# Optimization experiments

Hardware: AMD Instinct MI355X
Metric: run time of the kernel (lower is better)

Reference implementation:

```python
import jax, jax.numpy as jnp
import numpy as np

B, T, D, H = 256, 1024, 128, 256
SHIFT = 1


def setup_inputs() -> dict:
    key = jax.random.key(0)
    ks = jax.random.split(key, 16)

    def w(k, shp):
        return jax.random.normal(k, shp, dtype=jnp.float32) / np.float32(np.sqrt(shp[0]))

    return {
        "x": jax.random.normal(ks[0], (B, T, D), dtype=jnp.float32),
        "Wx": w(ks[1], (D, H)), "bx": jnp.zeros((H,), jnp.float32),
        "W1": w(ks[2], (D, 100)), "b1": jnp.zeros((100,), jnp.float32),
        "W2": w(ks[3], (100, 100)), "b2": jnp.zeros((100,), jnp.float32),
        "W3": w(ks[4], (100, 100)), "b3": jnp.zeros((100,), jnp.float32),
        "W4": w(ks[5], (100, 50)), "b4": jnp.zeros((50,), jnp.float32),
        "W5": w(ks[6], (50, H)), "b5": jnp.zeros((H,), jnp.float32),
        "Wo": w(ks[7], (H, 1)), "bo": jnp.zeros((1,), jnp.float32),
        "shift": SHIFT,
    }


def reference(x, Wx, bx, W1, b1, W2, b2, W3, b3, W4, b4, W5, b5, Wo, bo, shift):
    # x: [B, T, D] -> time-major [T, B, D] (matches input.permute(1,0,2))
    xs = jnp.swapaxes(x, 0, 1)
    # Input-dependent parts are independent of hidden state: batch them over time.
    lin_x = xs @ Wx + bx                       # [T, B, H]
    h = jax.nn.relu(xs @ W1 + b1)
    h = jax.nn.relu(h @ W2 + b2)
    h = jax.nn.relu(h @ W3 + b3)
    h = jax.nn.relu(h @ W4 + b4)
    fx = jax.nn.sigmoid(h @ W5 + b5)           # [T, B, H]
    gate = fx * jax.nn.sigmoid(lin_x)          # [T, B, H]

    def step(hid, bt):
        hid = jax.nn.relu(jnp.roll(hid, shift, axis=-1) + bt)
        return hid, None

    hidden0 = jnp.zeros((x.shape[0], Wx.shape[1]), dtype=x.dtype)
    hidden, _ = jax.lax.scan(step, hidden0, gate)
    output = jax.nn.sigmoid(hidden @ Wo + bo)  # [B, 1]
    return (output, hidden)
```

## Files before the change

### kernel.cpp

```cpp
#include <hip/hip_runtime.h>
#include <math.h>

#define B_N 256
#define T_N 1024
#define D_N 128
#define H_N 256

#define SPS 120

#define SP_OFF  0
#define SQ_OFF  7680
#define GUARD_OFF 15360
#define ACC_OFF 15368
#define SMEM_SH 15880

typedef __attribute__((ext_vector_type(8))) short short8;
typedef __attribute__((ext_vector_type(4))) float f32x4;

#define WXT_OFF 0
#define W1T_OFF 32768
#define W2T_OFF 47104
#define W3T_OFF 61440
#define W4T_OFF 75776
#define W5T_OFF 83968
#define WT_TOTAL 100352

__device__ __forceinline__ float sigmoid_f(float z) {
    return 1.0f / (1.0f + __expf(-z));
}
__device__ __forceinline__ unsigned short f2bf(float f) {
    unsigned u = __float_as_uint(f);
    return (unsigned short)((u + 0x7FFFu + ((u >> 16) & 1u)) >> 16);
}

__global__ __launch_bounds__(256) void prep_weights(
    const float* __restrict__ Wx, const float* __restrict__ W1,
    const float* __restrict__ W2, const float* __restrict__ W3,
    const float* __restrict__ W4, const float* __restrict__ W5,
    short* __restrict__ wt)
{
    int idx = blockIdx.x * 256 + threadIdx.x;
    if (idx >= WT_TOTAL) return;
    const float* src; int base, KR, K, N;
    if (idx < W1T_OFF)      { src = Wx; base = WXT_OFF; KR = 4; K = 128; N = 256; }
    else if (idx < W2T_OFF) { src = W1; base = W1T_OFF; KR = 4; K = 128; N = 100; }
    else if (idx < W3T_OFF) { src = W2; base = W2T_OFF; KR = 4; K = 100; N = 100; }
    else if (idx < W4T_OFF) { src = W3; base = W3T_OFF; KR = 4; K = 100; N = 100; }
    else if (idx < W5T_OFF) { src = W4; base = W4T_OFF; KR = 4; K = 100; N =  50; }
    else                    { src = W5; base = W5T_OFF; KR = 2; K =  50; N = 256; }
    int e    = idx - base;
    int j    = e & 7;
    int slot = e >> 3;
    int lane = slot & 63;
    int kk   = slot >> 6;
    int k4   = kk & (KR - 1);
    int nt   = kk / KR;
    int n = nt * 16 + (lane & 15);
    int k = k4 * 32 + (lane >> 4) * 8 + j;
    float v = (k < K && n < N) ? src[(size_t)k * N + n] : 0.0f;
    wt[idx] = (short)f2bf(v);
}

template<int STRIDE>
__device__ __forceinline__ void loadA(const short* __restrict__ base, short8 (&a)[4],
                                      int mbase, int lr, int lq)
{
    #pragma unroll
    for (int k = 0; k < 4; ++k)
        a[k] = *reinterpret_cast<const short8*>(&base[(mbase + lr) * STRIDE + k * 32 + lq * 8]);
}

template<int NT, int OUTS>
__device__ __forceinline__ void denseLG(const short8 (&a)[4], const short* __restrict__ gW,
                                        const float* __restrict__ bias, int ncap,
                                        short* __restrict__ dst, int mbase, int lr, int lq,
                                        int lane)
{
    #pragma unroll 2
    for (int nt = 0; nt < NT; ++nt) {
        const int n0 = nt * 16;
        f32x4 acc = {0.f, 0.f, 0.f, 0.f};
        #pragma unroll
        for (int k = 0; k < 4; ++k) {
            const short8 bf = *reinterpret_cast<const short8*>(&gW[((nt * 4 + k) * 64 + lane) * 8]);
            acc = __builtin_amdgcn_mfma_f32_16x16x32_bf16(a[k], bf, acc, 0, 0, 0);
        }
        const bool valid = (n0 + lr < ncap);
        const float bv = valid ? bias[n0 + lr] : 0.0f;
        #pragma unroll
        for (int r = 0; r < 4; ++r) {
            float v = valid ? fmaxf(acc[r] + bv, 0.0f) : 0.0f;
            dst[(mbase + lq * 4 + r) * OUTS + n0 + lr] = (short)f2bf(v);
        }
    }
}

__global__ __launch_bounds__(256, 4) void srnn_gate_scan(
    const float* __restrict__ x, const short* __restrict__ wt,
    const float* __restrict__ bx, const float* __restrict__ b1,
    const float* __restrict__ b2, const float* __restrict__ b3,
    const float* __restrict__ b4, const float* __restrict__ b5,
    const int* __restrict__ shiftp,
    float* __restrict__ out)
{
    __shared__ __align__(16) short smem[SMEM_SH];
    short* sP = smem + SP_OFF;
    short* sQ = smem + SQ_OFF;
    float* accum = reinterpret_cast<float*>(smem + ACC_OFF);

    const int tid  = threadIdx.x;
    const int b    = blockIdx.x & 255;
    const int seg  = blockIdx.x >> 8;
    const int lane = tid & 63;
    const int mbase = (tid >> 6) * 16;
    const int lr = lane & 15;
    const int lq = lane >> 4;
    const int s  = *shiftp;
    const int tw0 = seg * 64 + mbase;

    {
        const float4 z = {0.f, 0.f, 0.f, 0.f};
        float4* dst = reinterpret_cast<float4*>(smem);
        #pragma unroll
        for (int i = 0; i < 8; ++i) {
            int sl = tid + i * 256;
            if (sl < SMEM_SH / 8) dst[sl] = z;
        }
    }

    short8 ax4[4];
    {
        const float* xr = x + ((size_t)b * T_N + tw0 + lr) * D_N;
        #pragma unroll
        for (int k = 0; k < 4; ++k) {
            const float4 v0 = *reinterpret_cast<const float4*>(&xr[k * 32 + lq * 8]);
            const float4 v1 = *reinterpret_cast<const float4*>(&xr[k * 32 + lq * 8 + 4]);
            short8 t;
            t[0] = (short)f2bf(v0.x); t[1] = (short)f2bf(v0.y);
            t[2] = (short)f2bf(v0.z); t[3] = (short)f2bf(v0.w);
            t[4] = (short)f2bf(v1.x); t[5] = (short)f2bf(v1.y);
            t[6] = (short)f2bf(v1.z); t[7] = (short)f2bf(v1.w);
            ax4[k] = t;
        }
    }
    __syncthreads();

    short8 aL[4];
    denseLG<7, SPS>(ax4, wt + W1T_OFF, b1, 100, sP, mbase, lr, lq, lane);
    loadA<SPS>(sP, aL, mbase, lr, lq);
    denseLG<7, SPS>(aL, wt + W2T_OFF, b2, 100, sQ, mbase, lr, lq, lane);
    loadA<SPS>(sQ, aL, mbase, lr, lq);
    denseLG<7, SPS>(aL, wt + W3T_OFF, b3, 100, sP, mbase, lr, lq, lane);
    loadA<SPS>(sP, aL, mbase, lr, lq);
    denseLG<4, SPS>(aL, wt + W4T_OFF, b4, 50, sQ, mbase, lr, lq, lane);

    short8 c0 = *reinterpret_cast<const short8*>(&sQ[(mbase + lr) * SPS + 0 + lq * 8]);
    short8 c1 = *reinterpret_cast<const short8*>(&sQ[(mbase + lr) * SPS + 32 + lq * 8]);

    const short* gWx = wt + WXT_OFF;
    const short* gW5 = wt + W5T_OFF;
    #pragma unroll 2
    for (int ntl = 0; ntl < 16; ++ntl) {
        const int n0 = ntl * 16;
        f32x4 axv = {0.f, 0.f, 0.f, 0.f};
        #pragma unroll
        for (int k = 0; k < 4; ++k) {
            const short8 bf = *reinterpret_cast<const short8*>(&gWx[((ntl * 4 + k) * 64 + lane) * 8]);
            axv = __builtin_amdgcn_mfma_f32_16x16x32_bf16(ax4[k], bf, axv, 0, 0, 0);
        }
        f32x4 a5v = {0.f, 0.f, 0.f, 0.f};
        {
            const short8 bf0 = *reinterpret_cast<const short8*>(&gW5[((ntl * 2 + 0) * 64 + lane) * 8]);
            const short8 bf1 = *reinterpret_cast<const short8*>(&gW5[((ntl * 2 + 1) * 64 + lane) * 8]);
            a5v = __builtin_amdgcn_mfma_f32_16x16x32_bf16(c0, bf0, a5v, 0, 0, 0);
            a5v = __builtin_amdgcn_mfma_f32_16x16x32_bf16(c1, bf1, a5v, 0, 0, 0);
        }
        const float bxv = bx[n0 + lr];
        const float b5v = b5[n0 + lr];
        #pragma unroll
        for (int r = 0; r < 4; ++r) {
            const int t = tw0 + lq * 4 + r;
            const float g = sigmoid_f(a5v[r] + b5v) * sigmoid_f(axv[r] + bxv);
            int v = n0 + lr + s * (T_N - 1 - t);
            v %= H_N; if (v < 0) v += H_N;
            atomicAdd(&accum[v], g);
        }
    }
    __syncthreads();

    atomicAdd(&out[256 + b * 256 + tid], accum[tid]);
}

__global__ __launch_bounds__(256) void srnn_output(
    const float* __restrict__ Wo, const float* __restrict__ bo,
    float* __restrict__ out)
{
    __shared__ float red[256];
    const int b = blockIdx.x, tid = threadIdx.x;
    red[tid] = out[256 + b * 256 + tid] * Wo[tid];
    __syncthreads();
    #pragma unroll
    for (int off = 128; off > 0; off >>= 1) {
        if (tid < off) red[tid] += red[tid + off];
        __syncthreads();
    }
    if (tid == 0) out[b] = sigmoid_f(red[0] + bo[0]);
}

extern "C" void kernel_launch(void* const* d_in, const int* in_sizes, int n_in,
                              void* d_out, int out_size, void* d_ws, size_t ws_size,
                              hipStream_t stream)
{
    const float* x  = (const float*)d_in[0];
    const float* Wx = (const float*)d_in[1];
    const float* bx = (const float*)d_in[2];
    const float* W1 = (const float*)d_in[3];
    const float* b1 = (const float*)d_in[4];
    const float* W2 = (const float*)d_in[5];
    const float* b2 = (const float*)d_in[6];
    const float* W3 = (const float*)d_in[7];
    const float* b3 = (const float*)d_in[8];
    const float* W4 = (const float*)d_in[9];
    const float* b4 = (const float*)d_in[10];
    const float* W5 = (const float*)d_in[11];
    const float* b5 = (const float*)d_in[12];
    const float* Wo = (const float*)d_in[13];
    const float* bo = (const float*)d_in[14];
    const int* shiftp = (const int*)d_in[15];
    float* out = (float*)d_out;
    short* wt  = (short*)d_ws;

    hipMemsetAsync(d_out, 0, (size_t)out_size * sizeof(float), stream);

    prep_weights<<<dim3((WT_TOTAL + 255) / 256), dim3(256), 0, stream>>>(
        Wx, W1, W2, W3, W4, W5, wt);
    srnn_gate_scan<<<dim3(4096), dim3(256), 0, stream>>>(
        x, wt, bx, b1, b2, b3, b4, b5, shiftp, out);
    srnn_output<<<dim3(256), dim3(256), 0, stream>>>(Wo, bo, out);
}
```

Measured before the change: 576.5 us.

## Process two row tiles per wave, fuse output reduction, merge memset into prep

Each wave now handles 32 time rows, so every loaded weight fragment feeds two MFMAs. This halves weight-fragment traffic per row, and the grid is cut to 2048 blocks. The final Wo reduction moves into the scan kernel, where the last-arriving segment block per batch does it after a per-batch atomic counter. The output memset is folded into the weight-prep kernel. The sigmoid product is simplified to one reciprocal and the modulo to a mask. This adds register pressure, a counter in workspace, and a fence-based completion protocol.

New measurement: 699.3 us. 1.21x slower.

```diff
diff --git a/kernel.cpp b/kernel.cpp
--- a/kernel.cpp
+++ b/kernel.cpp
@@ -5,14 +5,12 @@
 #define T_N 1024
 #define D_N 128
 #define H_N 256
+#define NSEG 8
 
 #define SPS 120
-
-#define SP_OFF  0
-#define SQ_OFF  7680
-#define GUARD_OFF 15360
-#define ACC_OFF 15368
-#define SMEM_SH 15880
+#define SACT_SH (4 * 32 * SPS)
+#define ACC_OFF (SACT_SH + 8)
+#define SMEM_SH (ACC_OFF + 512)
 
 typedef __attribute__((ext_vector_type(8))) short short8;
 typedef __attribute__((ext_vector_type(4))) float f32x4;
@@ -33,13 +31,19 @@
     return (unsigned short)((u + 0x7FFFu + ((u >> 16) & 1u)) >> 16);
 }
 
-__global__ __launch_bounds__(256) void prep_weights(
+__global__ __launch_bounds__(256) void prep_init(
     const float* __restrict__ Wx, const float* __restrict__ W1,
     const float* __restrict__ W2, const float* __restrict__ W3,
     const float* __restrict__ W4, const float* __restrict__ W5,
-    short* __restrict__ wt)
+    short* __restrict__ wt, float* __restrict__ out, int* __restrict__ cnt)
 {
     int idx = blockIdx.x * 256 + threadIdx.x;
+    if (idx < 16448) {
+        const float4 z = {0.f, 0.f, 0.f, 0.f};
+        reinterpret_cast<float4*>(out)[idx] = z;
+    } else if (idx < 16448 + 256) {
+        cnt[idx - 16448] = 0;
+    }
     if (idx >= WT_TOTAL) return;
     const float* src; int base, KR, K, N;
     if (idx < W1T_OFF)      { src = Wx; base = WXT_OFF; KR = 4; K = 128; N = 256; }
@@ -61,36 +65,40 @@
     wt[idx] = (short)f2bf(v);
 }
 
-template<int STRIDE>
-__device__ __forceinline__ void loadA(const short* __restrict__ base, short8 (&a)[4],
-                                      int mbase, int lr, int lq)
-{
-    #pragma unroll
-    for (int k = 0; k < 4; ++k)
-        a[k] = *reinterpret_cast<const short8*>(&base[(mbase + lr) * STRIDE + k * 32 + lq * 8]);
-}
-
-template<int NT, int OUTS>
-__device__ __forceinline__ void denseLG(const short8 (&a)[4], const short* __restrict__ gW,
+__device__ __forceinline__ void loadA2(const short* __restrict__ sA, short8 (&a)[2][4],
+                                       int lr, int lq)
+{
+    #pragma unroll
+    for (int rb = 0; rb < 2; ++rb)
+        #pragma unroll
+        for (int k = 0; k < 4; ++k)
+            a[rb][k] = *reinterpret_cast<const short8*>(&sA[(rb * 16 + lr) * SPS + k * 32 + lq * 8]);
+}
+
+template<int NT>
+__device__ __forceinline__ void denseL2(const short8 (&a)[2][4], const short* __restrict__ gW,
                                         const float* __restrict__ bias, int ncap,
-                                        short* __restrict__ dst, int mbase, int lr, int lq,
-                                        int lane)
+                                        short* __restrict__ sA, int lr, int lq, int lane)
 {
     #pragma unroll 2
     for (int nt = 0; nt < NT; ++nt) {
         const int n0 = nt * 16;
-        f32x4 acc = {0.f, 0.f, 0.f, 0.f};
+        f32x4 acc0 = {0.f, 0.f, 0.f, 0.f};
+        f32x4 acc1 = {0.f, 0.f, 0.f, 0.f};
         #pragma unroll
         for (int k = 0; k < 4; ++k) {
             const short8 bf = *reinterpret_cast<const short8*>(&gW[((nt * 4 + k) * 64 + lane) * 8]);
-            acc = __builtin_amdgcn_mfma_f32_16x16x32_bf16(a[k], bf, acc, 0, 0, 0);
+            acc0 = __builtin_amdgcn_mfma_f32_16x16x32_bf16(a[0][k], bf, acc0, 0, 0, 0);
+            acc1 = __builtin_amdgcn_mfma_f32_16x16x32_bf16(a[1][k], bf, acc1, 0, 0, 0);
         }
         const bool valid = (n0 + lr < ncap);
         const float bv = valid ? bias[n0 + lr] : 0.0f;
         #pragma unroll
         for (int r = 0; r < 4; ++r) {
-            float v = valid ? fmaxf(acc[r] + bv, 0.0f) : 0.0f;
-            dst[(mbase + lq * 4 + r) * OUTS + n0 + lr] = (short)f2bf(v);
+            float v0 = valid ? fmaxf(acc0[r] + bv, 0.0f) : 0.0f;
+            float v1 = valid ? fmaxf(acc1[r] + bv, 0.0f) : 0.0f;
+            sA[(lq * 4 + r) * SPS + n0 + lr]        = (short)f2bf(v0);
+            sA[(16 + lq * 4 + r) * SPS + n0 + lr]   = (short)f2bf(v1);
         }
     }
 }
@@ -101,22 +109,23 @@
     const float* __restrict__ b2, const float* __restrict__ b3,
     const float* __restrict__ b4, const float* __restrict__ b5,
     const int* __restrict__ shiftp,
+    const float* __restrict__ Wo, const float* __restrict__ bo,
+    int* __restrict__ cnt,
     float* __restrict__ out)
 {
     __shared__ __align__(16) short smem[SMEM_SH];
-    short* sP = smem + SP_OFF;
-    short* sQ = smem + SQ_OFF;
     float* accum = reinterpret_cast<float*>(smem + ACC_OFF);
 
     const int tid  = threadIdx.x;
     const int b    = blockIdx.x & 255;
     const int seg  = blockIdx.x >> 8;
     const int lane = tid & 63;
-    const int mbase = (tid >> 6) * 16;
+    const int wid  = tid >> 6;
     const int lr = lane & 15;
     const int lq = lane >> 4;
     const int s  = *shiftp;
-    const int tw0 = seg * 64 + mbase;
+    const int tw0 = seg * 128 + wid * 32;
+    short* sA = smem + wid * 32 * SPS;
 
     {
         const float4 z = {0.f, 0.f, 0.f, 0.f};
@@ -128,9 +137,10 @@
         }
     }
 
-    short8 ax4[4];
-    {
-        const float* xr = x + ((size_t)b * T_N + tw0 + lr) * D_N;
+    short8 ax[2][4];
+    #pragma unroll
+    for (int rb = 0; rb < 2; ++rb) {
+        const float* xr = x + ((size_t)b * T_N + tw0 + rb * 16 + lr) * D_N;
         #pragma unroll
         for (int k = 0; k < 4; ++k) {
             const float4 v0 = *reinterpret_cast<const float4*>(&xr[k * 32 + lq * 8]);
@@ -140,71 +150,95 @@
             t[2] = (short)f2bf(v0.z); t[3] = (short)f2bf(v0.w);
             t[4] = (short)f2bf(v1.x); t[5] = (short)f2bf(v1.y);
             t[6] = (short)f2bf(v1.z); t[7] = (short)f2bf(v1.w);
-            ax4[k] = t;
-        }
-    }
-    __syncthreads();
-
-    short8 aL[4];
-    denseLG<7, SPS>(ax4, wt + W1T_OFF, b1, 100, sP, mbase, lr, lq, lane);
-    loadA<SPS>(sP, aL, mbase, lr, lq);
-    denseLG<7, SPS>(aL, wt + W2T_OFF, b2, 100, sQ, mbase, lr, lq, lane);
-    loadA<SPS>(sQ, aL, mbase, lr, lq);
-    denseLG<7, SPS>(aL, wt + W3T_OFF, b3, 100, sP, mbase, lr, lq, lane);
-    loadA<SPS>(sP, aL, mbase, lr, lq);
-    denseLG<4, SPS>(aL, wt + W4T_OFF, b4, 50, sQ, mbase, lr, lq, lane);
-
-    short8 c0 = *reinterpret_cast<const short8*>(&sQ[(mbase + lr) * SPS + 0 + lq * 8]);
-    short8 c1 = *reinterpret_cast<const short8*>(&sQ[(mbase + lr) * SPS + 32 + lq * 8]);
+            ax[rb][k] = t;
+        }
+    }
+    __syncthreads();
+
+    short8 aL[2][4];
+    denseL2<7>(ax, wt + W1T_OFF, b1, 100, sA, lr, lq, lane);
+    loadA2(sA, aL, lr, lq);
+    denseL2<7>(aL, wt + W2T_OFF, b2, 100, sA, lr, lq, lane);
+    loadA2(sA, aL, lr, lq);
+    denseL2<7>(aL, wt + W3T_OFF, b3, 100, sA, lr, lq, lane);
+    loadA2(sA, aL, lr, lq);
+    denseL2<4>(aL, wt + W4T_OFF, b4, 50, sA, lr, lq, lane);
+
+    short8 c[2][2];
+    #pragma unroll
+    for (int rb = 0; rb < 2; ++rb) {
+        c[rb][0] = *reinterpret_cast<const short8*>(&sA[(rb * 16 + lr) * SPS + 0 + lq * 8]);
+        c[rb][1] = *reinterpret_cast<const short8*>(&sA[(rb * 16 + lr) * SPS + 32 + lq * 8]);
+    }
 
     const short* gWx = wt + WXT_OFF;
     const short* gW5 = wt + W5T_OFF;
+    const int tbase = T_N - 1 - tw0;
     #pragma unroll 2
     for (int ntl = 0; ntl < 16; ++ntl) {
         const int n0 = ntl * 16;
-        f32x4 axv = {0.f, 0.f, 0.f, 0.f};
+        f32x4 axv0 = {0.f, 0.f, 0.f, 0.f};
+        f32x4 axv1 = {0.f, 0.f, 0.f, 0.f};
         #pragma unroll
         for (int k = 0; k < 4; ++k) {
             const short8 bf = *reinterpret_cast<const short8*>(&gWx[((ntl * 4 + k) * 64 + lane) * 8]);
-            axv = __builtin_amdgcn_mfma_f32_16x16x32_bf16(ax4[k], bf, axv, 0, 0, 0);
-        }
-        f32x4 a5v = {0.f, 0.f, 0.f, 0.f};
+            axv0 = __builtin_amdgcn_mfma_f32_16x16x32_bf16(ax[0][k], bf, axv0, 0, 0, 0);
+            axv1 = __builtin_amdgcn_mfma_f32_16x16x32_bf16(ax[1][k], bf, axv1, 0, 0, 0);
+        }
+        f32x4 a5v0 = {0.f, 0.f, 0.f, 0.f};
+        f32x4 a5v1 = {0.f, 0.f, 0.f, 0.f};
         {
             const short8 bf0 = *reinterpret_cast<const short8*>(&gW5[((ntl * 2 + 0) * 64 + lane) * 8]);
             const short8 bf1 = *reinterpret_cast<const short8*>(&gW5[((ntl * 2 + 1) * 64 + lane) * 8]);
-            a5v = __builtin_amdgcn_mfma_f32_16x16x32_bf16(c0, bf0, a5v, 0, 0, 0);
-            a5v = __builtin_amdgcn_mfma_f32_16x16x32_bf16(c1, bf1, a5v, 0, 0, 0);
+            a5v0 = __builtin_amdgcn_mfma_f32_16x16x32_bf16(c[0][0], bf0, a5v0, 0, 0, 0);
+            a5v1 = __builtin_amdgcn_mfma_f32_16x16x32_bf16(c[1][0], bf0, a5v1, 0, 0, 0);
+            a5v0 = __builtin_amdgcn_mfma_f32_16x16x32_bf16(c[0][1], bf1, a5v0, 0, 0, 0);
+            a5v1 = __builtin_amdgcn_mfma_f32_16x16x32_bf16(c[1][1], bf1, a5v1, 0, 0, 0);
         }
         const float bxv = bx[n0 + lr];
         const float b5v = b5[n0 + lr];
         #pragma unroll
-        for (int r = 0; r < 4; ++r) {
-            const int t = tw0 + lq * 4 + r;
-            const float g = sigmoid_f(a5v[r] + b5v) * sigmoid_f(axv[r] + bxv);
-            int v = n0 + lr + s * (T_N - 1 - t);
-            v %= H_N; if (v < 0) v += H_N;
-            atomicAdd(&accum[v], g);
+        for (int rb = 0; rb < 2; ++rb) {
+            const f32x4& axv = rb ? axv1 : axv0;
+            const f32x4& a5v = rb ? a5v1 : a5v0;
+            #pragma unroll
+            for (int r = 0; r < 4; ++r) {
+                const int toff = rb * 16 + lq * 4 + r;
+                const float ea = __expf(-(a5v[r] + b5v));
+                const float eb = __expf(-(axv[r] + bxv));
+                const float g = 1.0f / ((1.0f + ea) * (1.0f + eb));
+                const int h = (int)(((unsigned)(n0 + lr + s * (tbase - toff))) & 255u);
+                atomicAdd(&accum[h], g);
+            }
         }
     }
     __syncthreads();
 
     atomicAdd(&out[256 + b * 256 + tid], accum[tid]);
-}
-
-__global__ __launch_bounds__(256) void srnn_output(
-    const float* __restrict__ Wo, const float* __restrict__ bo,
-    float* __restrict__ out)
-{
-    __shared__ float red[256];
-    const int b = blockIdx.x, tid = threadIdx.x;
-    red[tid] = out[256 + b * 256 + tid] * Wo[tid];
+    __threadfence();
+    __syncthreads();
+
+    int* flag = reinterpret_cast<int*>(accum);
+    if (tid == 0) {
+        const int old = atomicAdd(&cnt[b], 1);
+        __threadfence();
+        flag[0] = (old == NSEG - 1) ? 1 : 0;
+    }
+    __syncthreads();
+    if (!flag[0]) return;
+
+    const float hv = __hip_atomic_load(&out[256 + b * 256 + tid],
+                                       __ATOMIC_RELAXED, __HIP_MEMORY_SCOPE_AGENT);
+    const float pv = hv * Wo[tid];
+    __syncthreads();
+    accum[tid] = pv;
     __syncthreads();
     #pragma unroll
     for (int off = 128; off > 0; off >>= 1) {
-        if (tid < off) red[tid] += red[tid + off];
+        if (tid < off) accum[tid] += accum[tid + off];
         __syncthreads();
     }
-    if (tid == 0) out[b] = sigmoid_f(red[0] + bo[0]);
+    if (tid == 0) out[b] = sigmoid_f(accum[0] + bo[0]);
 }
 
 extern "C" void kernel_launch(void* const* d_in, const int* in_sizes, int n_in,
@@ -229,12 +263,10 @@
     const int* shiftp = (const int*)d_in[15];
     float* out = (float*)d_out;
     short* wt  = (short*)d_ws;
-
-    hipMemsetAsync(d_out, 0, (size_t)out_size * sizeof(float), stream);
-
-    prep_weights<<<dim3((WT_TOTAL + 255) / 256), dim3(256), 0, stream>>>(
-        Wx, W1, W2, W3, W4, W5, wt);
-    srnn_gate_scan<<<dim3(4096), dim3(256), 0, stream>>>(
-        x, wt, bx, b1, b2, b3, b4, b5, shiftp, out);
-    srnn_output<<<dim3(256), dim3(256), 0, stream>>>(Wo, bo, out);
-}
+    int* cnt   = (int*)((char*)d_ws + WT_TOTAL * 2);
+
+    prep_init<<<dim3((WT_TOTAL + 255) / 256), dim3(256), 0, stream>>>(
+        Wx, W1, W2, W3, W4, W5, wt, out, cnt);
+    srnn_gate_scan<<<dim3(2048), dim3(256), 0, stream>>>(
+        x, wt, bx, b1, b2, b3, b4, b5, shiftp, Wo, bo, cnt, out);
+}
```
